# Performance work log

Measured on AMD Instinct MI355X. Metric: run time of the kernel, lower is better.

## Reference

```python
import jax, jax.numpy as jnp
import numpy as np

DEGREE = 3          # bspline_array passes t_dim positionally as degree
C_DIM = 64          # coefficients per spline
N_SPLINES = 64      # n
T_DIM = C_DIM + DEGREE + 1   # knots per spline = 68
BATCH = 65536


def setup_inputs() -> dict:
    key = jax.random.key(0)
    k1, k2, k3 = jax.random.split(key, 3)
    x = jax.random.normal(k1, (BATCH, N_SPLINES), dtype=jnp.float32)
    t = jax.random.normal(k2, (N_SPLINES, T_DIM), dtype=jnp.float32)   # knot vectors (learned, unsorted as in source)
    c = jax.random.normal(k3, (N_SPLINES, C_DIM), dtype=jnp.float32)   # control coefficients
    return {"x": x, "t": t, "c": c}


def _safe_div(num, den):
    # Cox-de Boor convention: 0/0 := 0 (handles repeated knots)
    zero = den == 0
    return jnp.where(zero, 0.0, num / jnp.where(zero, 1.0, den))


def cox_deboor_batched(t, c, x):
    """Vectorized Cox-de Boor over all n splines and the whole batch.

    t: [n, T_DIM] knots, c: [n, C_DIM] coeffs, x: [B, n] -> out [B, n]
    """
    xe = x[..., None]                                   # [B, n, 1]
    # degree-0 basis: indicator t_i <= x < t_{i+1}      # [B, n, T_DIM-1]
    N = ((t[:, :-1] <= xe) & (xe < t[:, 1:])).astype(x.dtype)
    for k in range(1, DEGREE + 1):
        m = T_DIM - 1 - k
        left = _safe_div(xe - t[:, :m], t[:, k:k + m] - t[:, :m]) * N[..., :m]
        right = _safe_div(t[:, k + 1:k + 1 + m] - xe,
                          t[:, k + 1:k + 1 + m] - t[:, 1:1 + m]) * N[..., 1:1 + m]
        N = left + right                                # [B, n, m]
    # S(x) = sum_i c_i * B_{i,p}(x)
    return jnp.einsum('bni,ni->bn', N[..., :C_DIM], c)  # [B, n]


def reference(x, t, c):
    return cox_deboor_batched(t, c, x)
```

## Files before the change

### kernel.cpp

```cpp
#include <hip/hip_runtime.h>

#define BATCH 65536
#define NSPL  64
#define CDIM  64
#define TDIM  68
#define QI    67
#define RTN   67

#define TCOLS 16
#define TROWS 128
#define NTHR  256
#define PITCH 129
#define KPAD  128


__global__ __launch_bounds__(128) void prep(const float* __restrict__ T,
                                            const float* __restrict__ C,
                                            float4* __restrict__ RT,
                                            float* __restrict__ SRT) {
    __shared__ double  td[TDIM];
    __shared__ double  cd[CDIM];
    __shared__ double  R1[QI], R2[TDIM - 2], R3[TDIM - 3];
    __shared__ double4 Qd[QI];
    __shared__ float   tf[TDIM];
    __shared__ float   srt[TDIM];

    const int s = blockIdx.x;
    const int t = threadIdx.x;

    if (t < TDIM) { float v = T[s * TDIM + t]; tf[t] = v; td[t] = (double)v; }
    if (t >= 64 && t < 64 + CDIM) cd[t - 64] = (double)C[s * CDIM + t - 64];
    __syncthreads();

    if (t < TDIM - 1) { double d = td[t + 1] - td[t]; R1[t] = (d == 0.0) ? 0.0 : 1.0 / d; }
    if (t < TDIM - 2) { double d = td[t + 2] - td[t]; R2[t] = (d == 0.0) ? 0.0 : 1.0 / d; }
    if (t < TDIM - 3) { double d = td[t + 3] - td[t]; R3[t] = (d == 0.0) ? 0.0 : 1.0 / d; }
    if (t < TDIM) {
        float v = tf[t];
        int r = 0;
        for (int k = 0; k < TDIM; ++k)
            r += (tf[k] < v) || (tf[k] == v && k < t);
        srt[r] = v;
    }
    __syncthreads();

    {
        float v = (t < TDIM) ? srt[t] : __builtin_huge_valf();
        SRT[s * KPAD + t] = v;
    }

    if (t < QI) {
        const int i = t;
        double q0 = 0, q1 = 0, q2 = 0, q3 = 0;
        for (int j = i - 3; j <= i; ++j) {
            if (j < 0 || j > CDIM - 1) continue;
            double cj = cd[j];
            for (int b2 = 0; b2 < 2; ++b2) {
                int m2 = j + b2;
                double D3 = R3[j + b2];
                double p3 = b2 ? -D3 : D3;
                double r3 = b2 ? D3 * td[j + 4] : -D3 * td[j];
                for (int b1 = 0; b1 < 2; ++b1) {
                    int m1 = m2 + b1;
                    double D2 = R2[m2 + b1];
                    double p2 = b1 ? -D2 : D2;
                    double r2 = b1 ? D2 * td[m2 + 3] : -D2 * td[m2];
                    for (int b0 = 0; b0 < 2; ++b0) {
                        if (m1 + b0 != i) continue;
                        double D1 = R1[m1 + b0];
                        double p1 = b0 ? -D1 : D1;
                        double r1 = b0 ? D1 * td[m1 + 2] : -D1 * td[m1];
                        double a2 = p3 * p2, a1 = p3 * r2 + r3 * p2, a0 = r3 * r2;
                        q3 += cj * (a2 * p1);
                        q2 += cj * (a2 * r1 + a1 * p1);
                        q1 += cj * (a1 * r1 + a0 * p1);
                        q0 += cj * (a0 * r1);
                    }
                }
            }
        }
        double4 q; q.x = q0; q.y = q1; q.z = q2; q.w = q3;
        Qd[i] = q;
    }
    __syncthreads();

    if (t >= 1 && t <= RTN) {
        const float xs = srt[t - 1];
        double a0 = 0, a1 = 0, a2 = 0, a3 = 0;
        for (int i = 0; i < QI; ++i) {
            if (tf[i] <= xs && xs < tf[i + 1]) {
                double4 q = Qd[i];
                a0 += q.x; a1 += q.y; a2 += q.z; a3 += q.w;
            }
        }
        float4 v; v.x = (float)a0; v.y = (float)a1; v.z = (float)a2; v.w = (float)a3;
        RT[s * RTN + (t - 1)] = v;
    }
}

__global__ __launch_bounds__(NTHR) void bspline_main(const float* __restrict__ X,
                                                     const float4* __restrict__ RT,
                                                     const float* __restrict__ SRT,
                                                     float* __restrict__ O) {
    __shared__ float xl[TCOLS * PITCH];
    __shared__ float ks[TCOLS * KPAD];

    const int tid  = threadIdx.x;
    const int lane = tid & 63;
    const int w    = tid >> 6;
    const int r0   = blockIdx.x * TROWS;
    const int s0   = blockIdx.y * TCOLS;

    {
        const float4* src = (const float4*)(SRT + s0 * KPAD);
        float4* dst = (float4*)ks;
        dst[tid]        = src[tid];
        dst[tid + NTHR] = src[tid + NTHR];
    }
    #pragma unroll
    for (int it = 0; it < 2; ++it) {
        int e = tid + it * NTHR;
        int r = e >> 2, q = e & 3;
        float4 v = *(const float4*)(X + (r0 + r) * NSPL + s0 + q * 4);
        xl[(q * 4 + 0) * PITCH + r] = v.x;
        xl[(q * 4 + 1) * PITCH + r] = v.y;
        xl[(q * 4 + 2) * PITCH + r] = v.z;
        xl[(q * 4 + 3) * PITCH + r] = v.w;
    }
    __syncthreads();

    #pragma unroll 1
    for (int cc = 0; cc < 4; ++cc) {
        const int c  = w * 4 + cc;
        const int sp = __builtin_amdgcn_readfirstlane(s0 + c);
        const float* kc = ks + c * KPAD;

        float* xc = xl + c * PITCH + lane;
        const float x0 = xc[0];
        const float x1 = xc[64];

        unsigned n0 = 0, n1 = 0;
        #pragma unroll
        for (int st = 64; st >= 1; st >>= 1) {
            float v0 = kc[n0 + st - 1];
            float v1 = kc[n1 + st - 1];
            n0 = (v0 <= x0) ? n0 + st : n0;
            n1 = (v1 <= x1) ? n1 + st : n1;
        }
        unsigned i0 = n0 - 1u; i0 = (i0 > 66u) ? 66u : i0;
        unsigned i1 = n1 - 1u; i1 = (i1 > 66u) ? 66u : i1;
        const float4* rts = RT + sp * RTN;
        float4 p0 = rts[i0];
        float4 p1 = rts[i1];
        float y0 = fmaf(fmaf(fmaf(p0.w, x0, p0.z), x0, p0.y), x0, p0.x);
        float y1 = fmaf(fmaf(fmaf(p1.w, x1, p1.z), x1, p1.y), x1, p1.x);
        y0 = (n0 - 1u < 67u) ? y0 : 0.f;
        y1 = (n1 - 1u < 67u) ? y1 : 0.f;
        xc[0]  = y0;
        xc[64] = y1;
    }
    __syncthreads();

    #pragma unroll
    for (int it = 0; it < 2; ++it) {
        int e = tid + it * NTHR;
        int r = e >> 2, q = e & 3;
        float4 v;
        v.x = xl[(q * 4 + 0) * PITCH + r];
        v.y = xl[(q * 4 + 1) * PITCH + r];
        v.z = xl[(q * 4 + 2) * PITCH + r];
        v.w = xl[(q * 4 + 3) * PITCH + r];
        *(float4*)(O + (r0 + r) * NSPL + s0 + q * 4) = v;
    }
}

extern "C" void kernel_launch(void* const* d_in, const int* in_sizes, int n_in,
                              void* d_out, int out_size, void* d_ws, size_t ws_size,
                              hipStream_t stream) {
    const float* X = (const float*)d_in[0];
    const float* T = (const float*)d_in[1];
    const float* C = (const float*)d_in[2];
    float* O = (float*)d_out;
    float4* RT = (float4*)d_ws;
    float* SRT = (float*)((char*)d_ws + NSPL * RTN * sizeof(float4));

    prep<<<NSPL, 128, 0, stream>>>(T, C, RT, SRT);
    dim3 grid(BATCH / TROWS, NSPL / TCOLS);
    bspline_main<<<grid, NTHR, 0, stream>>>(X, RT, SRT, O);
}
```

Measured before the change: 88.83 us.

## Drop LDS transpose, map threads to spline columns, register-cache top search pivots

The shared-memory staging and transpose of X and O is removed. Each thread now handles one spline column and reads and writes global memory directly with scalar, 16-float-wide row segments. The first three levels of the binary search over sorted knots now use pivot values cached in registers, and the knot table gets a padded LDS pitch (132) to spread bank accesses. An occupancy hint of 8 blocks is added. This trades vectorized float4 global accesses for fewer LDS round trips and barriers. Each RT lookup now gathers per lane across 16 splines instead of being uniform per wave.

```diff
diff --git a/kernel.cpp b/kernel.cpp
--- a/kernel.cpp
+++ b/kernel.cpp
@@ -10,8 +10,8 @@
 #define TCOLS 16
 #define TROWS 128
 #define NTHR  256
-#define PITCH 129
 #define KPAD  128
+#define KLDS  132
 
 
 __global__ __launch_bounds__(128) void prep(const float* __restrict__ T,
@@ -98,79 +98,78 @@
     }
 }
 
-__global__ __launch_bounds__(NTHR) void bspline_main(const float* __restrict__ X,
-                                                     const float4* __restrict__ RT,
-                                                     const float* __restrict__ SRT,
-                                                     float* __restrict__ O) {
-    __shared__ float xl[TCOLS * PITCH];
-    __shared__ float ks[TCOLS * KPAD];
+__global__ __launch_bounds__(NTHR, 8) void bspline_main(const float* __restrict__ X,
+                                                        const float4* __restrict__ RT,
+                                                        const float* __restrict__ SRT,
+                                                        float* __restrict__ O) {
+    __shared__ float ks[TCOLS * KLDS];
 
-    const int tid  = threadIdx.x;
-    const int lane = tid & 63;
-    const int w    = tid >> 6;
-    const int r0   = blockIdx.x * TROWS;
-    const int s0   = blockIdx.y * TCOLS;
+    const int tid = threadIdx.x;
+    const int r0  = blockIdx.x * TROWS;
+    const int s0  = blockIdx.y * TCOLS;
 
     {
         const float4* src = (const float4*)(SRT + s0 * KPAD);
-        float4* dst = (float4*)ks;
-        dst[tid]        = src[tid];
-        dst[tid + NTHR] = src[tid + NTHR];
-    }
-    #pragma unroll
-    for (int it = 0; it < 2; ++it) {
-        int e = tid + it * NTHR;
-        int r = e >> 2, q = e & 3;
-        float4 v = *(const float4*)(X + (r0 + r) * NSPL + s0 + q * 4);
-        xl[(q * 4 + 0) * PITCH + r] = v.x;
-        xl[(q * 4 + 1) * PITCH + r] = v.y;
-        xl[(q * 4 + 2) * PITCH + r] = v.z;
-        xl[(q * 4 + 3) * PITCH + r] = v.w;
+        #pragma unroll
+        for (int it = 0; it < 2; ++it) {
+            int e = tid + it * NTHR;
+            int c = e >> 5, p = e & 31;
+            float4 v = src[c * 32 + p];
+            *(float4*)(ks + c * KLDS + p * 4) = v;
+        }
     }
     __syncthreads();
 
-    #pragma unroll 1
-    for (int cc = 0; cc < 4; ++cc) {
-        const int c  = w * 4 + cc;
-        const int sp = __builtin_amdgcn_readfirstlane(s0 + c);
-        const float* kc = ks + c * KPAD;
+    const int c  = tid & 15;
+    const int rs = tid >> 4;
+    const float* kc = ks + c * KLDS;
 
-        float* xc = xl + c * PITCH + lane;
-        const float x0 = xc[0];
-        const float x1 = xc[64];
+    const float pv1  = kc[63];
+    const float pv2a = kc[31], pv2b = kc[95];
+    const float pv3a = kc[15], pv3b = kc[47], pv3c = kc[79], pv3d = kc[111];
 
-        unsigned n0 = 0, n1 = 0;
+    const float4* rts = RT + (s0 + c) * RTN;
+    const float*  xp  = X + (r0 + rs) * NSPL + s0 + c;
+    float*        op  = O + (r0 + rs) * NSPL + s0 + c;
+
+    #pragma unroll
+    for (int j = 0; j < 4; ++j) {
+        const int ra = (32 * j) * NSPL, rb = (32 * j + 16) * NSPL;
+        const float x0 = xp[ra];
+        const float x1 = xp[rb];
+
+        unsigned n0 = (pv1 <= x0) ? 64u : 0u;
+        unsigned n1 = (pv1 <= x1) ? 64u : 0u;
+        float q0 = n0 ? pv2b : pv2a;
+        float q1 = n1 ? pv2b : pv2a;
+        n0 += (q0 <= x0) ? 32u : 0u;
+        n1 += (q1 <= x1) ? 32u : 0u;
+        float a0 = (n0 & 32u) ? pv3b : pv3a;
+        float b0 = (n0 & 32u) ? pv3d : pv3c;
+        float a1 = (n1 & 32u) ? pv3b : pv3a;
+        float b1 = (n1 & 32u) ? pv3d : pv3c;
+        float r0v = (n0 & 64u) ? b0 : a0;
+        float r1v = (n1 & 64u) ? b1 : a1;
+        n0 += (r0v <= x0) ? 16u : 0u;
+        n1 += (r1v <= x1) ? 16u : 0u;
         #pragma unroll
-        for (int st = 64; st >= 1; st >>= 1) {
+        for (int st = 8; st >= 1; st >>= 1) {
             float v0 = kc[n0 + st - 1];
             float v1 = kc[n1 + st - 1];
             n0 = (v0 <= x0) ? n0 + st : n0;
             n1 = (v1 <= x1) ? n1 + st : n1;
         }
+
         unsigned i0 = n0 - 1u; i0 = (i0 > 66u) ? 66u : i0;
         unsigned i1 = n1 - 1u; i1 = (i1 > 66u) ? 66u : i1;
-        const float4* rts = RT + sp * RTN;
         float4 p0 = rts[i0];
         float4 p1 = rts[i1];
         float y0 = fmaf(fmaf(fmaf(p0.w, x0, p0.z), x0, p0.y), x0, p0.x);
         float y1 = fmaf(fmaf(fmaf(p1.w, x1, p1.z), x1, p1.y), x1, p1.x);
         y0 = (n0 - 1u < 67u) ? y0 : 0.f;
         y1 = (n1 - 1u < 67u) ? y1 : 0.f;
-        xc[0]  = y0;
-        xc[64] = y1;
-    }
-    __syncthreads();
-
-    #pragma unroll
-    for (int it = 0; it < 2; ++it) {
-        int e = tid + it * NTHR;
-        int r = e >> 2, q = e & 3;
-        float4 v;
-        v.x = xl[(q * 4 + 0) * PITCH + r];
-        v.y = xl[(q * 4 + 1) * PITCH + r];
-        v.z = xl[(q * 4 + 2) * PITCH + r];
-        v.w = xl[(q * 4 + 3) * PITCH + r];
-        *(float4*)(O + (r0 + r) * NSPL + s0 + q * 4) = v;
+        op[ra] = y0;
+        op[rb] = y1;
     }
 }
 
```

After: 88.32 us, median of 2. About the same (-0.6%).
